# Kernel optimization log

Measured on AMD Instinct MI355X. Metric: run time of the kernel, lower is better.

Reference implementation:

```python
import jax, jax.numpy as jnp
import numpy as np

B, D = 32, 512
N_IMG, N_KN = 50000, 8192
C = 32          # num_classes
R = 16          # image_retrieval_number
K = 8           # knowledge_retrieval_number
NEG = -1e9


def setup_inputs() -> dict:
    key = jax.random.key(0)
    k1, k2, k3, k4, k5 = jax.random.split(key, 5)
    return {
        'query_embeddings': jax.random.normal(k1, (B, D), dtype=jnp.float32),
        'all_image_embeddings': jax.random.normal(k2, (N_IMG, D), dtype=jnp.float32),
        'all_knowledge_embeddings': jax.random.normal(k3, (N_KN, D), dtype=jnp.float32),
        'image_labels': jax.random.randint(k4, (N_IMG,), 0, C, dtype=jnp.int32),
        'knowledge_labels': jax.random.randint(k5, (N_KN,), 0, C, dtype=jnp.int32),
    }


def reference(query_embeddings, all_image_embeddings, all_knowledge_embeddings,
              image_labels, knowledge_labels):
    classes = jnp.arange(C, dtype=jnp.int32)
    img_class_mask = image_labels[None, :] == classes[:, None]       # [C, N_img]
    kn_class_mask = knowledge_labels[None, :] == classes[:, None]    # [C, N_kn]

    # per-class masked similarity retrieval of images
    sims = query_embeddings @ all_image_embeddings.T                 # [B, N_img]
    masked = jnp.where(img_class_mask[None], sims[:, None, :], NEG)  # [B, C, N_img]
    img_vals, img_idx = jax.lax.top_k(masked, R)                     # [B, C, R]
    img_w = jax.nn.softmax(img_vals, axis=-1)
    similar_images = all_image_embeddings[img_idx]                   # [B, C, R, D]

    # image fusion (average of query and attention-weighted retrieved context)
    fused_img = jnp.einsum('bcr,bcrd->bcd', img_w, similar_images)
    enhanced_images = 0.5 * (query_embeddings[:, None, :] + fused_img)  # [B, C, D]

    # class-masked knowledge retrieval for every retrieved image
    ksims = jnp.einsum('bcrd,nd->bcrn', similar_images, all_knowledge_embeddings)
    kmasked = jnp.where(kn_class_mask[None, :, None, :], ksims, NEG)  # [B, C, R, N_kn]
    k_vals, k_idx = jax.lax.top_k(kmasked, K)                         # [B, C, R, K]
    k_w = jax.nn.softmax(k_vals, axis=-1)
    selected_knowledge = all_knowledge_embeddings[k_idx]              # [B, C, R, K, D]

    # knowledge fusion: weight over K, then over R with image weights, average w/ query
    fused_k = jnp.einsum('bcrk,bcrkd->bcrd', k_w, selected_knowledge)
    fused_k = jnp.einsum('bcr,bcrd->bcd', img_w, fused_k)
    enhanced_knowledge = 0.5 * (query_embeddings[:, None, :] + fused_k)  # [B, C, D]

    return enhanced_images, enhanced_knowledge
```

## Files before the change

### kernel.cpp

```cpp
#include <hip/hip_runtime.h>
#include <math.h>

#define NIMG 50000
#define NKN  8192
#define BB   32
#define DD   512
#define CC   32
#define RR   16
#define KK   8
#define MMAX 384
#define SPLIT 4
#define SD4  (DD / 4 / SPLIT)

typedef float f2v __attribute__((ext_vector_type(2)));

__global__ __launch_bounds__(256) void build_lists(const int* __restrict__ labels,
                                                   int n, int* __restrict__ cnt,
                                                   int* __restrict__ list, int stride) {
    int i = blockIdx.x * 256 + threadIdx.x;
    if (i < n) {
        int c = labels[i];
        int pos = atomicAdd(&cnt[c], 1);
        list[c * stride + pos] = i;
    }
}

__global__ __launch_bounds__(256, 2) void sims_kernel(const float* __restrict__ Q,
                                                      const float* __restrict__ I,
                                                      float* __restrict__ SP) {
    int slice = blockIdx.y, tid = threadIdx.x;
    __shared__ float4 qs[BB][SD4];
    for (int i = tid; i < BB * SD4; i += 256) {
        int b = i / SD4, d = i % SD4;
        qs[b][d] = ((const float4*)Q)[b * (DD / 4) + slice * SD4 + d];
    }
    __syncthreads();

    int n0 = blockIdx.x * 512 + tid;
    int n1 = n0 + 256;
    bool v1ok = n1 < NIMG;
    int n1c = v1ok ? n1 : 0;

    float a0[BB], a1[BB];
#pragma unroll
    for (int b = 0; b < BB; b++) { a0[b] = 0.f; a1[b] = 0.f; }

    const float4* r0 = (const float4*)(I + (size_t)n0 * DD) + slice * SD4;
    const float4* r1 = (const float4*)(I + (size_t)n1c * DD) + slice * SD4;
    for (int d = 0; d < SD4; d++) {
        float4 x0 = r0[d], x1 = r1[d];
#pragma unroll
        for (int b = 0; b < BB; b++) {
            float4 q = qs[b][d];
            a0[b] += x0.x * q.x + x0.y * q.y + x0.z * q.z + x0.w * q.w;
            a1[b] += x1.x * q.x + x1.y * q.y + x1.z * q.z + x1.w * q.w;
        }
    }
    float* out = SP + (size_t)slice * BB * NIMG;
#pragma unroll
    for (int b = 0; b < BB; b++) {
        out[(size_t)b * NIMG + n0] = a0[b];
        if (v1ok) out[(size_t)b * NIMG + n1] = a1[b];
    }
}

__global__ __launch_bounds__(256) void combine_s(float4* __restrict__ SP) {
    int i = blockIdx.x * 256 + threadIdx.x;
    const int n4 = BB * NIMG / 4;
    if (i >= n4) return;
    float4 s0 = SP[i], s1 = SP[i + n4], s2 = SP[i + 2 * n4], s3 = SP[i + 3 * n4];
    float4 r;
    r.x = ((s0.x + s1.x) + s2.x) + s3.x;
    r.y = ((s0.y + s1.y) + s2.y) + s3.y;
    r.z = ((s0.z + s1.z) + s2.z) + s3.z;
    r.w = ((s0.w + s1.w) + s2.w) + s3.w;
    SP[i] = r;
}

__global__ __launch_bounds__(256) void topk_img(const float* __restrict__ S,
                                                const int* __restrict__ cnt,
                                                const int* __restrict__ list,
                                                int* __restrict__ t_idx,
                                                float* __restrict__ t_w) {
    int c = blockIdx.x, b = blockIdx.y, tid = threadIdx.x;
    int wave = tid >> 6, lane = tid & 63;
    __shared__ float wv_s[4];
    __shared__ int   wi_s[4];
    __shared__ float kv_s[RR];
    __shared__ int   ki_s[RR];

    int m = cnt[c];
    const float* Sb = S + (size_t)b * NIMG;

    float cv0, cv1, cv2, cv3, cv4, cv5, cv6;
    int   ci0, ci1, ci2, ci3, ci4, ci5, ci6;
#define LOADC(t) { int j = tid + t * 256; \
        if (j < m) { int n = list[c * NIMG + j]; cv##t = Sb[n]; ci##t = n; } \
        else { cv##t = -1e30f; ci##t = 0x7fffffff; } }
    LOADC(0) LOADC(1) LOADC(2) LOADC(3) LOADC(4) LOADC(5) LOADC(6)
#undef LOADC

    unsigned used = 0;
#define CANDT(t) { if (!(used & (1u << t)) && \
                       (cv##t > mv || (cv##t == mv && ci##t < mj))) \
                   { mv = cv##t; mj = ci##t; mt = t; } }
#define RND(k) { \
        float mv = -1e30f; int mj = 0x7fffffff; int mt = -1; \
        CANDT(0) CANDT(1) CANDT(2) CANDT(3) CANDT(4) CANDT(5) CANDT(6) \
        int lmj = mj; \
        for (int off = 32; off > 0; off >>= 1) { \
            float ov = __shfl_xor(mv, off); \
            int   oj = __shfl_xor(mj, off); \
            if (ov > mv || (ov == mv && oj < mj)) { mv = ov; mj = oj; } \
        } \
        if (lane == 0) { wv_s[wave] = mv; wi_s[wave] = mj; } \
        __syncthreads(); \
        float gv = wv_s[0]; int gj = wi_s[0]; \
        if (wv_s[1] > gv || (wv_s[1] == gv && wi_s[1] < gj)) { gv = wv_s[1]; gj = wi_s[1]; } \
        if (wv_s[2] > gv || (wv_s[2] == gv && wi_s[2] < gj)) { gv = wv_s[2]; gj = wi_s[2]; } \
        if (wv_s[3] > gv || (wv_s[3] == gv && wi_s[3] < gj)) { gv = wv_s[3]; gj = wi_s[3]; } \
        if (mt >= 0 && lmj == gj && lmj != 0x7fffffff) used |= (1u << mt); \
        if (tid == 0) { kv_s[k] = gv; ki_s[k] = gj; } \
        __syncthreads(); }

    RND(0)  RND(1)  RND(2)  RND(3)  RND(4)  RND(5)  RND(6)  RND(7)
    RND(8)  RND(9)  RND(10) RND(11) RND(12) RND(13) RND(14) RND(15)
#undef RND
#undef CANDT

    if (tid == 0) {
        float mx = kv_s[0], s = 0.f, e[RR];
#pragma unroll
        for (int k = 0; k < RR; k++) { e[k] = expf(kv_s[k] - mx); s += e[k]; }
        float inv = 1.f / s;
        size_t o = ((size_t)(b * CC) + c) * RR;
#pragma unroll
        for (int k = 0; k < RR; k++) { t_w[o + k] = e[k] * inv; t_idx[o + k] = ki_s[k]; }
    }
}

__global__ __launch_bounds__(256) void img_kernel(const float* __restrict__ Q,
                                                  const float* __restrict__ I,
                                                  const int* __restrict__ t_idx,
                                                  const float* __restrict__ t_w,
                                                  float* __restrict__ out) {
    int c = blockIdx.x, b = blockIdx.y, tid = threadIdx.x;
    __shared__ float w[RR];
    __shared__ int   id[RR];
    if (tid < RR) {
        size_t o = ((size_t)(b * CC) + c) * RR;
        w[tid] = t_w[o + tid]; id[tid] = t_idx[o + tid];
    }
    __syncthreads();
    for (int d = tid; d < DD; d += 256) {
        float acc = 0.f;
#pragma unroll
        for (int r = 0; r < RR; r++) acc += w[r] * I[(size_t)id[r] * DD + d];
        out[((size_t)(b * CC) + c) * DD + d] = 0.5f * (Q[b * DD + d] + acc);
    }
}

__global__ __launch_bounds__(256) void transpose_kn(const float* __restrict__ KN,
                                                    const int* __restrict__ kcnt,
                                                    const int* __restrict__ klist,
                                                    float4* __restrict__ KT4) {
    int c = blockIdx.x;
    int w = threadIdx.x >> 6, lane = threadIdx.x & 63;
    int j = blockIdx.y * 4 + w;
    int m = kcnt[c]; if (m > MMAX) m = MMAX;
    int row = klist[c * NKN + (j < m ? j : 0)];
    const float4* src = (const float4*)(KN + (size_t)row * DD);
    float4* dst = KT4 + (size_t)c * (DD / 4) * MMAX;
    float4 v0 = src[lane], v1 = src[lane + 64];
    dst[(size_t)lane * MMAX + j]        = v0;
    dst[(size_t)(lane + 64) * MMAX + j] = v1;
}

__global__ __launch_bounds__(512, 8) void knowledge_kernel(const float* __restrict__ Q,
                                                           const float* __restrict__ I,
                                                           const float* __restrict__ KN,
                                                           const float4* __restrict__ KT4,
                                                           const int* __restrict__ kcnt,
                                                           const int* __restrict__ klist,
                                                           const int* __restrict__ t_idx,
                                                           const float* __restrict__ t_w,
                                                           float* __restrict__ outk) {
    int c = blockIdx.x, b = blockIdx.y;
    int tid = threadIdx.x, wave = tid >> 6, lane = tid & 63;
    int rbase = wave * 2;

    __shared__ float  s_iw[RR];
    __shared__ int    s_ii[RR];
    __shared__ float  wgt[RR][KK];
    __shared__ int    kidx[RR][KK];

    if (tid < RR) {
        size_t o = ((size_t)(b * CC) + c) * RR;
        s_iw[tid] = t_w[o + tid]; s_ii[tid] = t_idx[o + tid];
    }
    __syncthreads();

    int i0 = __builtin_amdgcn_readfirstlane(s_ii[rbase + 0]);
    int i1 = __builtin_amdgcn_readfirstlane(s_ii[rbase + 1]);
    const float4* U0 = (const float4*)(I + (size_t)i0 * DD);
    const float4* U1 = (const float4*)(I + (size_t)i1 * DD);

    int m = kcnt[c]; if (m > MMAX) m = MMAX;
    int ng = (m + 63) >> 6;
    const float4* KTc = KT4 + (size_t)c * (DD / 4) * MMAX;

    f2v A0 = 0.f, A1 = 0.f, A2 = 0.f, A3 = 0.f, A4 = 0.f, A5 = 0.f;

#define LG(g) float4 kk##g = p[g * 64];
#define FG(g, rr) A##g[rr] = fmaf(kk##g.x, u.x, fmaf(kk##g.y, u.y, \
                   fmaf(kk##g.z, u.z, fmaf(kk##g.w, u.w, A##g[rr]))));
#define RRBLK(rr, FMAS) { float4 u = U##rr[d4]; FMAS }
#define SCORE(LOADS, F0, F1) \
        for (int d4 = 0; d4 < DD / 4; d4++) { \
            const float4* p = KTc + (size_t)d4 * MMAX + lane; \
            LOADS \
            RRBLK(0, F0) RRBLK(1, F1) }

    if (ng <= 4) {
        SCORE(LG(0) LG(1) LG(2) LG(3),
              FG(0,0) FG(1,0) FG(2,0) FG(3,0),
              FG(0,1) FG(1,1) FG(2,1) FG(3,1))
    } else if (ng == 5) {
        SCORE(LG(0) LG(1) LG(2) LG(3) LG(4),
              FG(0,0) FG(1,0) FG(2,0) FG(3,0) FG(4,0),
              FG(0,1) FG(1,1) FG(2,1) FG(3,1) FG(4,1))
    } else {
        SCORE(LG(0) LG(1) LG(2) LG(3) LG(4) LG(5),
              FG(0,0) FG(1,0) FG(2,0) FG(3,0) FG(4,0) FG(5,0),
              FG(0,1) FG(1,1) FG(2,1) FG(3,1) FG(4,1) FG(5,1))
    }
#undef SCORE
#undef RRBLK
#undef FG
#undef LG

#define CAND(t) { if (!(used & (1u << t)) && \
                      (lv##t > mv || (lv##t == mv && (t * 64 + lane) < mj))) \
                  { mv = lv##t; mj = t * 64 + lane; mt = t; } }

#define ROUND(k) { \
        float mv = -1e30f; int mj = 0x7fffffff; int mt = -1; \
        CAND(0) CAND(1) CAND(2) CAND(3) CAND(4) CAND(5) \
        int cj = mj; \
        for (int off = 32; off > 0; off >>= 1) { \
            float ov = __shfl_xor(mv, off); \
            int   oj = __shfl_xor(mj, off); \
            if (ov > mv || (ov == mv && oj < mj)) { mv = ov; mj = oj; } \
        } \
        if (cj == mj && mt >= 0) used |= (1u << mt); \
        if (lane == k) myj = mj; \
        kv##k = mv; }

#define TOPK_RR(rr) { \
        int r = rbase + rr; \
        float lv0 = (0 * 64 + lane < m) ? A0[rr] : -1e30f; \
        float lv1 = (1 * 64 + lane < m) ? A1[rr] : -1e30f; \
        float lv2 = (2 * 64 + lane < m) ? A2[rr] : -1e30f; \
        float lv3 = (3 * 64 + lane < m) ? A3[rr] : -1e30f; \
        float lv4 = (4 * 64 + lane < m) ? A4[rr] : -1e30f; \
        float lv5 = (5 * 64 + lane < m) ? A5[rr] : -1e30f; \
        unsigned used = 0; int myj = 0; \
        float kv0, kv1, kv2, kv3, kv4, kv5, kv6, kv7; \
        ROUND(0) ROUND(1) ROUND(2) ROUND(3) \
        ROUND(4) ROUND(5) ROUND(6) ROUND(7) \
        if (lane < KK) kidx[r][lane] = klist[c * NKN + myj]; \
        if (lane == 0) { \
            float e0 = 1.f; \
            float e1 = expf(kv1 - kv0), e2 = expf(kv2 - kv0), e3 = expf(kv3 - kv0); \
            float e4 = expf(kv4 - kv0), e5 = expf(kv5 - kv0), e6 = expf(kv6 - kv0); \
            float e7 = expf(kv7 - kv0); \
            float s = e0 + e1 + e2 + e3 + e4 + e5 + e6 + e7; \
            float wr = s_iw[r] / s; \
            wgt[r][0] = e0 * wr; wgt[r][1] = e1 * wr; wgt[r][2] = e2 * wr; \
            wgt[r][3] = e3 * wr; wgt[r][4] = e4 * wr; wgt[r][5] = e5 * wr; \
            wgt[r][6] = e6 * wr; wgt[r][7] = e7 * wr; \
        } }

    TOPK_RR(0) TOPK_RR(1)
#undef TOPK_RR
#undef ROUND
#undef CAND

    __syncthreads();

    float acc0 = 0.f;
#pragma unroll 8
    for (int p = 0; p < RR * KK; p++) {
        int r = p >> 3, k = p & 7;
        float w = wgt[r][k];
        acc0 += w * KN[(size_t)kidx[r][k] * DD + tid];
    }
    size_t o = ((size_t)(b * CC) + c) * DD;
    outk[o + tid] = 0.5f * (Q[b * DD + tid] + acc0);
}

extern "C" void kernel_launch(void* const* d_in, const int* in_sizes, int n_in,
                              void* d_out, int out_size, void* d_ws, size_t ws_size,
                              hipStream_t stream) {
    const float* Q  = (const float*)d_in[0];
    const float* I  = (const float*)d_in[1];
    const float* KN = (const float*)d_in[2];
    const int* ilab = (const int*)d_in[3];
    const int* klab = (const int*)d_in[4];

    char* ws = (char*)d_ws;
    float* SP       = (float*)ws;  ws += (size_t)SPLIT * BB * NIMG * 4;
    int*   img_list = (int*)ws;    ws += (size_t)CC * NIMG * 4;
    int*   kn_list  = (int*)ws;    ws += (size_t)CC * NKN * 4;
    int*   t_idx    = (int*)ws;    ws += (size_t)BB * CC * RR * 4;
    float* t_w      = (float*)ws;  ws += (size_t)BB * CC * RR * 4;
    int*   img_cnt  = (int*)ws;    ws += CC * 4;
    int*   kn_cnt   = (int*)ws;    ws += CC * 4;
    ws = (char*)(((size_t)ws + 255) & ~(size_t)255);
    float4* KT4     = (float4*)ws; ws += (size_t)CC * (DD / 4) * MMAX * 16;

    float* out_img = (float*)d_out;
    float* out_kn  = out_img + (size_t)BB * CC * DD;

    hipMemsetAsync(img_cnt, 0, 2 * CC * 4, stream);

    build_lists<<<(NIMG + 255) / 256, 256, 0, stream>>>(ilab, NIMG, img_cnt, img_list, NIMG);
    build_lists<<<(NKN  + 255) / 256, 256, 0, stream>>>(klab, NKN,  kn_cnt,  kn_list,  NKN);
    transpose_kn<<<dim3(CC, MMAX / 4), 256, 0, stream>>>(KN, kn_cnt, kn_list, KT4);
    sims_kernel<<<dim3((NIMG + 511) / 512, SPLIT), 256, 0, stream>>>(Q, I, SP);
    combine_s<<<(BB * NIMG / 4 + 255) / 256, 256, 0, stream>>>((float4*)SP);
    topk_img<<<dim3(CC, BB), 256, 0, stream>>>(SP, img_cnt, img_list, t_idx, t_w);
    img_kernel<<<dim3(CC, BB), 256, 0, stream>>>(Q, I, t_idx, t_w, (float*)d_out);
    knowledge_kernel<<<dim3(CC, BB), 512, 0, stream>>>(Q, I, KN, KT4, kn_cnt, kn_list, t_idx, t_w, out_kn);
}
```

Baseline: 417.3 us.

## Split knowledge scoring across wave pairs with 4 rows each and merge partial top-k

Each wave now handles four retrieved images over half of the class's knowledge candidate groups, rather than two images over all groups. Every loaded knowledge float4 is therefore reused across four image rows, which halves knowledge-matrix loads per FMA. The two half-wave top-8 lists per row are written to shared memory, and one lane merges them before computing the softmax weights. The change adds an extra barrier and a serial merge on a single lane. It also puts more accumulators in flight, which may raise register pressure under launch_bounds(512,8).

```diff
diff --git a/kernel.cpp b/kernel.cpp
--- a/kernel.cpp
+++ b/kernel.cpp
@@ -12,7 +12,7 @@
 #define SPLIT 4
 #define SD4  (DD / 4 / SPLIT)
 
-typedef float f2v __attribute__((ext_vector_type(2)));
+typedef float f4v __attribute__((ext_vector_type(4)));
 
 __global__ __launch_bounds__(256) void build_lists(const int* __restrict__ labels,
                                                    int n, int* __restrict__ cnt,
@@ -187,12 +187,16 @@
                                                            float* __restrict__ outk) {
     int c = blockIdx.x, b = blockIdx.y;
     int tid = threadIdx.x, wave = tid >> 6, lane = tid & 63;
-    int rbase = wave * 2;
+    int jhalf = wave & 1, rquad = wave >> 1;
+    int rbase = rquad * 4;
+    int g0 = jhalf, g1 = jhalf + 2, g2 = jhalf + 4;
 
     __shared__ float  s_iw[RR];
     __shared__ int    s_ii[RR];
     __shared__ float  wgt[RR][KK];
     __shared__ int    kidx[RR][KK];
+    __shared__ float  part_v[RR][2][KK];
+    __shared__ int    part_j[RR][2][KK];
 
     if (tid < RR) {
         size_t o = ((size_t)(b * CC) + c) * RR;
@@ -202,50 +206,60 @@
 
     int i0 = __builtin_amdgcn_readfirstlane(s_ii[rbase + 0]);
     int i1 = __builtin_amdgcn_readfirstlane(s_ii[rbase + 1]);
+    int i2 = __builtin_amdgcn_readfirstlane(s_ii[rbase + 2]);
+    int i3 = __builtin_amdgcn_readfirstlane(s_ii[rbase + 3]);
     const float4* U0 = (const float4*)(I + (size_t)i0 * DD);
     const float4* U1 = (const float4*)(I + (size_t)i1 * DD);
+    const float4* U2 = (const float4*)(I + (size_t)i2 * DD);
+    const float4* U3 = (const float4*)(I + (size_t)i3 * DD);
 
     int m = kcnt[c]; if (m > MMAX) m = MMAX;
     int ng = (m + 63) >> 6;
+    int nga = (g0 < ng) + (g1 < ng) + (g2 < ng);
     const float4* KTc = KT4 + (size_t)c * (DD / 4) * MMAX;
 
-    f2v A0 = 0.f, A1 = 0.f, A2 = 0.f, A3 = 0.f, A4 = 0.f, A5 = 0.f;
-
-#define LG(g) float4 kk##g = p[g * 64];
-#define FG(g, rr) A##g[rr] = fmaf(kk##g.x, u.x, fmaf(kk##g.y, u.y, \
-                   fmaf(kk##g.z, u.z, fmaf(kk##g.w, u.w, A##g[rr]))));
-#define RRBLK(rr, FMAS) { float4 u = U##rr[d4]; FMAS }
-#define SCORE(LOADS, F0, F1) \
-        for (int d4 = 0; d4 < DD / 4; d4++) { \
-            const float4* p = KTc + (size_t)d4 * MMAX + lane; \
-            LOADS \
-            RRBLK(0, F0) RRBLK(1, F1) }
-
-    if (ng <= 4) {
-        SCORE(LG(0) LG(1) LG(2) LG(3),
-              FG(0,0) FG(1,0) FG(2,0) FG(3,0),
-              FG(0,1) FG(1,1) FG(2,1) FG(3,1))
-    } else if (ng == 5) {
-        SCORE(LG(0) LG(1) LG(2) LG(3) LG(4),
-              FG(0,0) FG(1,0) FG(2,0) FG(3,0) FG(4,0),
-              FG(0,1) FG(1,1) FG(2,1) FG(3,1) FG(4,1))
-    } else {
-        SCORE(LG(0) LG(1) LG(2) LG(3) LG(4) LG(5),
-              FG(0,0) FG(1,0) FG(2,0) FG(3,0) FG(4,0) FG(5,0),
-              FG(0,1) FG(1,1) FG(2,1) FG(3,1) FG(4,1) FG(5,1))
-    }
-#undef SCORE
-#undef RRBLK
+    f4v A0 = 0.f, A1 = 0.f, A2 = 0.f;
+
+#define FG(gs, rr) A##gs[rr] = fmaf(k##gs.x, u.x, fmaf(k##gs.y, u.y, \
+                    fmaf(k##gs.z, u.z, fmaf(k##gs.w, u.w, A##gs[rr]))));
+
+    if (nga == 3) {
+        for (int d4 = 0; d4 < DD / 4; d4++) {
+            const float4* p = KTc + (size_t)d4 * MMAX + lane;
+            float4 k0 = p[g0 * 64], k1 = p[g1 * 64], k2 = p[g2 * 64];
+            { float4 u = U0[d4]; FG(0,0) FG(1,0) FG(2,0) }
+            { float4 u = U1[d4]; FG(0,1) FG(1,1) FG(2,1) }
+            { float4 u = U2[d4]; FG(0,2) FG(1,2) FG(2,2) }
+            { float4 u = U3[d4]; FG(0,3) FG(1,3) FG(2,3) }
+        }
+    } else if (nga == 2) {
+        for (int d4 = 0; d4 < DD / 4; d4++) {
+            const float4* p = KTc + (size_t)d4 * MMAX + lane;
+            float4 k0 = p[g0 * 64], k1 = p[g1 * 64];
+            { float4 u = U0[d4]; FG(0,0) FG(1,0) }
+            { float4 u = U1[d4]; FG(0,1) FG(1,1) }
+            { float4 u = U2[d4]; FG(0,2) FG(1,2) }
+            { float4 u = U3[d4]; FG(0,3) FG(1,3) }
+        }
+    } else if (nga == 1) {
+        for (int d4 = 0; d4 < DD / 4; d4++) {
+            const float4* p = KTc + (size_t)d4 * MMAX + lane;
+            float4 k0 = p[g0 * 64];
+            { float4 u = U0[d4]; FG(0,0) }
+            { float4 u = U1[d4]; FG(0,1) }
+            { float4 u = U2[d4]; FG(0,2) }
+            { float4 u = U3[d4]; FG(0,3) }
+        }
+    }
 #undef FG
-#undef LG
 
 #define CAND(t) { if (!(used & (1u << t)) && \
-                      (lv##t > mv || (lv##t == mv && (t * 64 + lane) < mj))) \
-                  { mv = lv##t; mj = t * 64 + lane; mt = t; } }
+                      (lv##t > mv || (lv##t == mv && jj##t < mj))) \
+                  { mv = lv##t; mj = jj##t; mt = t; } }
 
 #define ROUND(k) { \
         float mv = -1e30f; int mj = 0x7fffffff; int mt = -1; \
-        CAND(0) CAND(1) CAND(2) CAND(3) CAND(4) CAND(5) \
+        CAND(0) CAND(1) CAND(2) \
         int cj = mj; \
         for (int off = 32; off > 0; off >>= 1) { \
             float ov = __shfl_xor(mv, off); \
@@ -253,38 +267,50 @@
             if (ov > mv || (ov == mv && oj < mj)) { mv = ov; mj = oj; } \
         } \
         if (cj == mj && mt >= 0) used |= (1u << mt); \
-        if (lane == k) myj = mj; \
-        kv##k = mv; }
+        if (lane == k) { pv = mv; pj = mj; } }
 
 #define TOPK_RR(rr) { \
         int r = rbase + rr; \
-        float lv0 = (0 * 64 + lane < m) ? A0[rr] : -1e30f; \
-        float lv1 = (1 * 64 + lane < m) ? A1[rr] : -1e30f; \
-        float lv2 = (2 * 64 + lane < m) ? A2[rr] : -1e30f; \
-        float lv3 = (3 * 64 + lane < m) ? A3[rr] : -1e30f; \
-        float lv4 = (4 * 64 + lane < m) ? A4[rr] : -1e30f; \
-        float lv5 = (5 * 64 + lane < m) ? A5[rr] : -1e30f; \
-        unsigned used = 0; int myj = 0; \
-        float kv0, kv1, kv2, kv3, kv4, kv5, kv6, kv7; \
+        int jj0 = g0 * 64 + lane, jj1 = g1 * 64 + lane, jj2 = g2 * 64 + lane; \
+        float lv0 = (jj0 < m) ? A0[rr] : -1e30f; \
+        float lv1 = (jj1 < m) ? A1[rr] : -1e30f; \
+        float lv2 = (jj2 < m) ? A2[rr] : -1e30f; \
+        unsigned used = 0; float pv = -1e30f; int pj = 0x7fffffff; \
         ROUND(0) ROUND(1) ROUND(2) ROUND(3) \
         ROUND(4) ROUND(5) ROUND(6) ROUND(7) \
-        if (lane < KK) kidx[r][lane] = klist[c * NKN + myj]; \
-        if (lane == 0) { \
-            float e0 = 1.f; \
-            float e1 = expf(kv1 - kv0), e2 = expf(kv2 - kv0), e3 = expf(kv3 - kv0); \
-            float e4 = expf(kv4 - kv0), e5 = expf(kv5 - kv0), e6 = expf(kv6 - kv0); \
-            float e7 = expf(kv7 - kv0); \
-            float s = e0 + e1 + e2 + e3 + e4 + e5 + e6 + e7; \
-            float wr = s_iw[r] / s; \
-            wgt[r][0] = e0 * wr; wgt[r][1] = e1 * wr; wgt[r][2] = e2 * wr; \
-            wgt[r][3] = e3 * wr; wgt[r][4] = e4 * wr; wgt[r][5] = e5 * wr; \
-            wgt[r][6] = e6 * wr; wgt[r][7] = e7 * wr; \
-        } }
-
-    TOPK_RR(0) TOPK_RR(1)
+        if (lane < KK) { part_v[r][jhalf][lane] = pv; part_j[r][jhalf][lane] = pj; } }
+
+    TOPK_RR(0) TOPK_RR(1) TOPK_RR(2) TOPK_RR(3)
 #undef TOPK_RR
 #undef ROUND
 #undef CAND
+
+    __syncthreads();
+
+#define PICK(k) { float va = part_v[r][0][ia], vb = part_v[r][1][ib]; \
+                  int ja = part_j[r][0][ia], jb = part_j[r][1][ib]; \
+                  bool ta = (va > vb) || (va == vb && ja < jb); \
+                  mv##k = ta ? va : vb; int mjk = ta ? ja : jb; \
+                  kidx[r][k] = klist[c * NKN + (mjk == 0x7fffffff ? 0 : mjk)]; \
+                  ia += ta ? 1 : 0; ib += ta ? 0 : 1; }
+    if (jhalf == 0 && lane == 0) {
+        for (int rr = 0; rr < 4; rr++) {
+            int r = rbase + rr;
+            int ia = 0, ib = 0;
+            float mv0, mv1, mv2, mv3, mv4, mv5, mv6, mv7;
+            PICK(0) PICK(1) PICK(2) PICK(3) PICK(4) PICK(5) PICK(6) PICK(7)
+            float e0 = 1.f;
+            float e1 = expf(mv1 - mv0), e2 = expf(mv2 - mv0), e3 = expf(mv3 - mv0);
+            float e4 = expf(mv4 - mv0), e5 = expf(mv5 - mv0), e6 = expf(mv6 - mv0);
+            float e7 = expf(mv7 - mv0);
+            float s = e0 + e1 + e2 + e3 + e4 + e5 + e6 + e7;
+            float wr = s_iw[r] / s;
+            wgt[r][0] = e0 * wr; wgt[r][1] = e1 * wr; wgt[r][2] = e2 * wr;
+            wgt[r][3] = e3 * wr; wgt[r][4] = e4 * wr; wgt[r][5] = e5 * wr;
+            wgt[r][6] = e6 * wr; wgt[r][7] = e7 * wr;
+        }
+    }
+#undef PICK
 
     __syncthreads();
 
```

New measurement: 375.7 us. -10.0%, faster.
